# Kernel tuning notes

Hardware: AMD Instinct MI355X
Metric: run time of the kernel (lower is better)

## Reference

```python
import jax, jax.numpy as jnp
import numpy as np

NEG = -1e32
EPS_LN = 1e-5

def _layer_norm(x, w, b):
    mu = jnp.mean(x, axis=-1, keepdims=True)
    var = jnp.mean((x - mu) ** 2, axis=-1, keepdims=True)
    return (x - mu) / jnp.sqrt(var + EPS_LN) * w + b

def setup_inputs() -> dict:
    key = jax.random.key(0)
    ks = jax.random.split(key, 10)
    B, S, D, H, F = 2, 2048, 1024, 16, 4096
    s = 0.02
    return {
        "query": jax.random.normal(ks[0], (B, S, D), jnp.float32),
        "key": jax.random.normal(ks[1], (B, S, D), jnp.float32),
        "values": jax.random.normal(ks[2], (B, S, D), jnp.float32),
        "Wk": jax.random.normal(ks[3], (D, D), jnp.float32) * s,
        "bk": jnp.zeros((D,), jnp.float32),
        "Wv": jax.random.normal(ks[4], (D, D), jnp.float32) * s,
        "bv": jnp.zeros((D,), jnp.float32),
        "Wo": jax.random.normal(ks[5], (D, D), jnp.float32) * s,
        "bo": jnp.zeros((D,), jnp.float32),
        "gammas": jax.random.normal(ks[6], (H, 1, 1), jnp.float32),
        "ln1_w": jnp.ones((D,), jnp.float32),
        "ln1_b": jnp.zeros((D,), jnp.float32),
        "W1": jax.random.normal(ks[7], (F, D), jnp.float32) * s,
        "b1": jnp.zeros((F,), jnp.float32),
        "W2": jax.random.normal(ks[8], (D, F), jnp.float32) * s,
        "b2": jnp.zeros((D,), jnp.float32),
        "ln2_w": jnp.ones((D,), jnp.float32),
        "ln2_b": jnp.zeros((D,), jnp.float32),
        "mask": 1,
    }

def _forward(query, key, values, Wk, bk, Wv, bv, Wo, bo, gammas,
             ln1_w, ln1_b, W1, b1, W2, b2, ln2_w, ln2_b, mask):
    B, S, D = query.shape
    H = gammas.shape[0]
    dk = D // H
    # kq_same=True: q and k both use k_linear
    def proj(x, W, b):
        return (x @ W.T + b).reshape(B, S, H, dk).transpose(0, 2, 1, 3)  # bhsd
    q = proj(query, Wk, bk)
    k = proj(key, Wk, bk)
    v = proj(values, Wv, bv)

    scores = jnp.einsum("bhqd,bhkd->bhqk", q, k) / np.sqrt(dk).astype(np.float32)
    # src_mask: np.triu(ones, k=mask)==0 -> allowed where j <= i + mask - 1
    allow = jnp.tril(jnp.ones((S, S), bool), k=mask - 1)[None, None]  # (1,1,S,S)

    # --- distance decay (no_grad block in torch) ---
    scores_ = jax.nn.softmax(jnp.where(allow, scores, NEG), axis=-1)
    scores_ = scores_ * allow.astype(scores_.dtype)
    distcum = jnp.cumsum(scores_, axis=-1)
    disttotal = jnp.sum(scores_, axis=-1, keepdims=True)
    idx = jnp.arange(S)
    position_effect = jnp.abs(idx[:, None] - idx[None, :]).astype(jnp.float32)[None, None]
    dist_scores = jnp.sqrt(jnp.clip((disttotal - distcum) * position_effect, 0.0, None))
    gamma = -jax.nn.softplus(gammas)[None]  # (1,H,1,1)
    total_effect = jnp.clip(jnp.exp(dist_scores * gamma), 1e-5, 1e5)
    total_effect = jax.lax.stop_gradient(total_effect)
    # ---

    scores = scores * total_effect
    scores = jnp.where(allow, scores, NEG)
    attn = jax.nn.softmax(scores, axis=-1)
    out = jnp.einsum("bhqk,bhkd->bhqd", attn, v)
    concat = out.transpose(0, 2, 1, 3).reshape(B, S, D)
    query2 = concat @ Wo.T + bo

    x = _layer_norm(query + query2, ln1_w, ln1_b)
    ff = jax.nn.relu(x @ W1.T + b1) @ W2.T + b2
    x = _layer_norm(x + ff, ln2_w, ln2_b)
    return x

def reference(query, key, values, Wk, bk, Wv, bv, Wo, bo, gammas,
              ln1_w, ln1_b, W1, b1, W2, b2, ln2_w, ln2_b, mask):
    return _forward(query, key, values, Wk, bk, Wv, bv, Wo, bo, gammas,
                    ln1_w, ln1_b, W1, b1, W2, b2, ln2_w, ln2_b, mask)
```

## Files before the change

### kernel.cpp

```cpp
#include <hip/hip_runtime.h>
#include <hip/hip_bf16.h>

#define B_   2
#define S_   2048
#define D_   1024
#define H_   16
#define DK_  64
#define F_   4096
#define M_   (B_*S_)
#define PD   72

typedef __attribute__((ext_vector_type(8))) short short8;
typedef __attribute__((ext_vector_type(4))) float f32x4;

__device__ __forceinline__ float bf2f(unsigned short s) { return __uint_as_float(((unsigned int)s) << 16); }
__device__ __forceinline__ unsigned short f2bf(float f) {
    unsigned int u = __float_as_uint(f);
    u += 0x7fffu + ((u >> 16) & 1u);
    return (unsigned short)(u >> 16);
}

__device__ __forceinline__ bool probe_f32(const unsigned int* p) {
    return *p == 0x3F800000u;
}
__device__ __forceinline__ float ld1e(const void* p, size_t idx, bool f32) {
    return f32 ? ((const float*)p)[idx] : bf2f(((const unsigned short*)p)[idx]);
}
__device__ __forceinline__ void st1e(void* p, size_t idx, bool f32, float v) {
    if (f32) ((float*)p)[idx] = v;
    else     ((unsigned short*)p)[idx] = f2bf(v);
}

__device__ __forceinline__ void async16(void* lds, const void* g) {
    __builtin_amdgcn_global_load_lds(
        (const __attribute__((address_space(1))) void*)g,
        (__attribute__((address_space(3))) void*)lds, 16, 0, 0);
}

__device__ __forceinline__ unsigned int cvt_pk_bf16(float a, float b) {
    unsigned int r;
    asm("v_cvt_pk_bf16_f32 %0, %1, %2" : "=v"(r) : "v"(a), "v"(b));
    return r;
}

template <bool IS_MAX>
__device__ __forceinline__ float block_reduce(float val, float* buf, int tid) {
    buf[tid] = val;
    __syncthreads();
    #pragma unroll
    for (int off = 128; off > 0; off >>= 1) {
        if (tid < off) {
            float o = buf[tid + off];
            buf[tid] = IS_MAX ? fmaxf(buf[tid], o) : (buf[tid] + o);
        }
        __syncthreads();
    }
    float r = buf[0];
    __syncthreads();
    return r;
}

__global__ __launch_bounds__(256) void cvt_all(
    const void* __restrict__ W1, const void* __restrict__ W2,
    const void* __restrict__ Wk, const void* __restrict__ Wv,
    const void* __restrict__ Wo,
    const void* __restrict__ Qi, const void* __restrict__ Ki,
    const void* __restrict__ Vi,
    unsigned short* __restrict__ W1b, unsigned short* __restrict__ W2b,
    unsigned short* __restrict__ Wkb, unsigned short* __restrict__ Wvb,
    unsigned short* __restrict__ Wob,
    unsigned short* __restrict__ qcb, unsigned short* __restrict__ kcb,
    unsigned short* __restrict__ vcb,
    const unsigned int* __restrict__ probe)
{
    const bool p32 = probe_f32(probe);
    const int blk = blockIdx.x;
    const void* src;
    unsigned short* dst;
    int off;
    if (blk < 2048)      { src = W1; dst = W1b; off = blk; }
    else if (blk < 4096) { src = W2; dst = W2b; off = blk - 2048; }
    else if (blk < 4608) { src = Wk; dst = Wkb; off = blk - 4096; }
    else if (blk < 5120) { src = Wv; dst = Wvb; off = blk - 4608; }
    else if (blk < 5632) { src = Wo; dst = Wob; off = blk - 5120; }
    else if (blk < 7680) { if (!p32) return; src = Qi; dst = qcb; off = blk - 5632; }
    else if (blk < 9728) { if (!p32) return; src = Ki; dst = kcb; off = blk - 7680; }
    else                 { if (!p32) return; src = Vi; dst = vcb; off = blk - 9728; }
    const int i8 = (off * 256 + threadIdx.x) * 8;
    if (p32) {
        const float4 a = *(const float4*)((const float*)src + i8);
        const float4 b = *(const float4*)((const float*)src + i8 + 4);
        short8 o;
        o[0] = (short)f2bf(a.x); o[1] = (short)f2bf(a.y);
        o[2] = (short)f2bf(a.z); o[3] = (short)f2bf(a.w);
        o[4] = (short)f2bf(b.x); o[5] = (short)f2bf(b.y);
        o[6] = (short)f2bf(b.z); o[7] = (short)f2bf(b.w);
        *(short8*)(dst + i8) = o;
    } else {
        *(uint4*)(dst + i8) = *(const uint4*)((const unsigned short*)src + i8);
    }
}

template <int RELU, int AEXT, int CEXT>
__device__ __forceinline__ void gemm_body(
    const void* __restrict__ A,
    const unsigned short* __restrict__ W,
    const void* __restrict__ bias,
    void* __restrict__ C,
    int M, int N, int K, bool p32, int bx, int by)
{
    __shared__ unsigned short As[2][128 * 32];
    __shared__ unsigned short Ws[2][128 * 32];

    const bool a32 = AEXT && p32;
    const bool c32 = CEXT && p32;

    const int tid = threadIdx.x;
    const int lane = tid & 63;
    const int w = tid >> 6;
    const int wr = w >> 1;
    const int wc = w & 1;
    const int col16 = lane & 15;
    const int quad = lane >> 4;

    const int m0 = by * 128;
    const int n0 = bx * 128;

    const int c0 = tid, c1 = 256 + tid;
    const int r0 = c0 >> 2, kc0 = (((c0 & 3) ^ ((c0 >> 3) & 3)) * 8);
    const int r1 = c1 >> 2, kc1 = (((c1 & 3) ^ ((c1 >> 3) & 3)) * 8);

    const int fcol = ((quad ^ ((col16 >> 1) & 3)) * 8);

    f32x4 acc[4][4];
    #pragma unroll
    for (int mt = 0; mt < 4; mt++)
        #pragma unroll
        for (int nt = 0; nt < 4; nt++)
            acc[mt][nt] = (f32x4){0.f, 0.f, 0.f, 0.f};

    auto stage = [&](int bb, int k0) {
        async16(&Ws[bb][c0 * 8], W + (size_t)(n0 + r0) * K + k0 + kc0);
        async16(&Ws[bb][c1 * 8], W + (size_t)(n0 + r1) * K + k0 + kc1);
        if (a32) {
            const float* a0 = (const float*)A + (size_t)(m0 + r0) * K + k0 + kc0;
            const float* a1 = (const float*)A + (size_t)(m0 + r1) * K + k0 + kc1;
            const float4 x0 = *(const float4*)a0, y0 = *(const float4*)(a0 + 4);
            const float4 x1 = *(const float4*)a1, y1 = *(const float4*)(a1 + 4);
            short8 s0, s1;
            s0[0] = (short)f2bf(x0.x); s0[1] = (short)f2bf(x0.y);
            s0[2] = (short)f2bf(x0.z); s0[3] = (short)f2bf(x0.w);
            s0[4] = (short)f2bf(y0.x); s0[5] = (short)f2bf(y0.y);
            s0[6] = (short)f2bf(y0.z); s0[7] = (short)f2bf(y0.w);
            s1[0] = (short)f2bf(x1.x); s1[1] = (short)f2bf(x1.y);
            s1[2] = (short)f2bf(x1.z); s1[3] = (short)f2bf(x1.w);
            s1[4] = (short)f2bf(y1.x); s1[5] = (short)f2bf(y1.y);
            s1[6] = (short)f2bf(y1.z); s1[7] = (short)f2bf(y1.w);
            *(short8*)&As[bb][c0 * 8] = s0;
            *(short8*)&As[bb][c1 * 8] = s1;
        } else {
            const unsigned short* Ab = (const unsigned short*)A;
            async16(&As[bb][c0 * 8], Ab + (size_t)(m0 + r0) * K + k0 + kc0);
            async16(&As[bb][c1 * 8], Ab + (size_t)(m0 + r1) * K + k0 + kc1);
        }
    };

    stage(0, 0);
    __syncthreads();
    int cur = 0;
    for (int k0 = 0; k0 < K; k0 += 32) {
        const int nxt = cur ^ 1;
        if (k0 + 32 < K) stage(nxt, k0 + 32);

        short8 av[4], bv[4];
        #pragma unroll
        for (int mt = 0; mt < 4; mt++)
            av[mt] = *(const short8*)&As[cur][(wr * 64 + mt * 16 + col16) * 32 + fcol];
        #pragma unroll
        for (int nt = 0; nt < 4; nt++)
            bv[nt] = *(const short8*)&Ws[cur][(wc * 64 + nt * 16 + col16) * 32 + fcol];
        #pragma unroll
        for (int mt = 0; mt < 4; mt++)
            #pragma unroll
            for (int nt = 0; nt < 4; nt++)
                acc[mt][nt] = __builtin_amdgcn_mfma_f32_16x16x32_bf16(
                    av[mt], bv[nt], acc[mt][nt], 0, 0, 0);
        __syncthreads();
        cur = nxt;
    }

    #pragma unroll
    for (int mt = 0; mt < 4; mt++) {
        const int row = m0 + wr * 64 + mt * 16 + quad * 4;
        #pragma unroll
        for (int nt = 0; nt < 4; nt++) {
            const int col = n0 + wc * 64 + nt * 16 + col16;
            const float bb = ld1e(bias, col, p32);
            #pragma unroll
            for (int r = 0; r < 4; r++) {
                float v = acc[mt][nt][r] + bb;
                if (RELU) v = fmaxf(v, 0.f);
                st1e(C, (size_t)(row + r) * N + col, c32, v);
            }
        }
    }
}

template <int RELU, int AEXT, int CEXT>
__global__ __launch_bounds__(256) void gemm_mf(
    const void* __restrict__ A,
    const unsigned short* __restrict__ W,
    const void* __restrict__ bias,
    void* __restrict__ C,
    int M, int N, int K,
    const unsigned int* __restrict__ probe)
{
    gemm_body<RELU, AEXT, CEXT>(A, W, bias, C, M, N, K, probe_f32(probe),
                                blockIdx.x, blockIdx.y);
}

template <int RELU, int CEXT>
__global__ __launch_bounds__(1024) void gemm_sk(
    const unsigned short* __restrict__ A,
    const unsigned short* __restrict__ W,
    const void* __restrict__ bias,
    void* __restrict__ C,
    int M, int N, int K,
    const unsigned int* __restrict__ probe)
{
    __shared__ unsigned short SS[4][2][2][128 * 32];
    float* const R0 = (float*)&SS[0][0][0][0];
    float* const R1 = (float*)&SS[2][0][0][0];

    const bool p32 = probe_f32(probe);
    const bool c32 = CEXT && p32;

    const int tid = threadIdx.x;
    const int g = tid >> 8;
    const int tl = tid & 255;
    const int lane = tl & 63;
    const int w = tl >> 6;
    const int wr = w >> 1;
    const int wc = w & 1;
    const int col16 = lane & 15;
    const int quad = lane >> 4;

    const int m0 = blockIdx.y * 128;
    const int n0 = blockIdx.x * 128;

    const int c0 = tl, c1 = 256 + tl;
    const int r0 = c0 >> 2, kc0 = (((c0 & 3) ^ ((c0 >> 3) & 3)) * 8);
    const int r1 = c1 >> 2, kc1 = (((c1 & 3) ^ ((c1 >> 3) & 3)) * 8);
    const int fcol = ((quad ^ ((col16 >> 1) & 3)) * 8);

    const int Kq = K >> 2;
    const int kbeg = g * Kq;

    f32x4 acc[4][4];
    #pragma unroll
    for (int mt = 0; mt < 4; mt++)
        #pragma unroll
        for (int nt = 0; nt < 4; nt++)
            acc[mt][nt] = (f32x4){0.f, 0.f, 0.f, 0.f};

    auto stage = [&](int bb, int k0) {
        async16(&SS[g][bb][1][c0 * 8], W + (size_t)(n0 + r0) * K + k0 + kc0);
        async16(&SS[g][bb][1][c1 * 8], W + (size_t)(n0 + r1) * K + k0 + kc1);
        async16(&SS[g][bb][0][c0 * 8], A + (size_t)(m0 + r0) * K + k0 + kc0);
        async16(&SS[g][bb][0][c1 * 8], A + (size_t)(m0 + r1) * K + k0 + kc1);
    };

    stage(0, kbeg);
    __syncthreads();
    int cur = 0;
    for (int kk = 0; kk < Kq; kk += 32) {
        const int nxt = cur ^ 1;
        if (kk + 32 < Kq) stage(nxt, kbeg + kk + 32);

        short8 av[4], bv[4];
        #pragma unroll
        for (int mt = 0; mt < 4; mt++)
            av[mt] = *(const short8*)&SS[g][cur][0][(wr * 64 + mt * 16 + col16) * 32 + fcol];
        #pragma unroll
        for (int nt = 0; nt < 4; nt++)
            bv[nt] = *(const short8*)&SS[g][cur][1][(wc * 64 + nt * 16 + col16) * 32 + fcol];
        #pragma unroll
        for (int mt = 0; mt < 4; mt++)
            #pragma unroll
            for (int nt = 0; nt < 4; nt++)
                acc[mt][nt] = __builtin_amdgcn_mfma_f32_16x16x32_bf16(
                    av[mt], bv[nt], acc[mt][nt], 0, 0, 0);
        __syncthreads();
        cur = nxt;
    }

    if (g == 1 || g == 3) {
        float* R = (g == 1) ? R0 : R1;
        #pragma unroll
        for (int mt = 0; mt < 4; mt++)
            #pragma unroll
            for (int nt = 0; nt < 4; nt++) {
                const int lrow = wr * 64 + mt * 16 + quad * 4;
                const int lcol = wc * 64 + nt * 16 + col16;
                #pragma unroll
                for (int r = 0; r < 4; r++)
                    R[(lrow + r) * 128 + lcol] = acc[mt][nt][r];
            }
    }
    __syncthreads();
    if (g == 0 || g == 2) {
        const float* R = (g == 0) ? R0 : R1;
        #pragma unroll
        for (int mt = 0; mt < 4; mt++)
            #pragma unroll
            for (int nt = 0; nt < 4; nt++) {
                const int lrow = wr * 64 + mt * 16 + quad * 4;
                const int lcol = wc * 64 + nt * 16 + col16;
                #pragma unroll
                for (int r = 0; r < 4; r++)
                    acc[mt][nt][r] += R[(lrow + r) * 128 + lcol];
            }
    }
    __syncthreads();
    if (g == 2) {
        #pragma unroll
        for (int mt = 0; mt < 4; mt++)
            #pragma unroll
            for (int nt = 0; nt < 4; nt++) {
                const int lrow = wr * 64 + mt * 16 + quad * 4;
                const int lcol = wc * 64 + nt * 16 + col16;
                #pragma unroll
                for (int r = 0; r < 4; r++)
                    R0[(lrow + r) * 128 + lcol] = acc[mt][nt][r];
            }
    }
    __syncthreads();
    if (g == 0) {
        #pragma unroll
        for (int mt = 0; mt < 4; mt++) {
            const int lrow = wr * 64 + mt * 16 + quad * 4;
            const int row = m0 + lrow;
            #pragma unroll
            for (int nt = 0; nt < 4; nt++) {
                const int lcol = wc * 64 + nt * 16 + col16;
                const int col = n0 + lcol;
                const float bb = ld1e(bias, col, p32);
                #pragma unroll
                for (int r = 0; r < 4; r++) {
                    float v = acc[mt][nt][r] + R0[(lrow + r) * 128 + lcol] + bb;
                    if (RELU) v = fmaxf(v, 0.f);
                    st1e(C, (size_t)(row + r) * N + col, c32, v);
                }
            }
        }
    }
}

__global__ __launch_bounds__(256) void gemm_proj(
    const void* __restrict__ q_orig, const void* __restrict__ k_orig,
    const void* __restrict__ v_orig,
    const unsigned short* __restrict__ qcb, const unsigned short* __restrict__ kcb,
    const unsigned short* __restrict__ vcb,
    const unsigned short* __restrict__ Wkb, const unsigned short* __restrict__ Wvb,
    const void* __restrict__ bk, const void* __restrict__ bv,
    unsigned short* __restrict__ qw, unsigned short* __restrict__ kw,
    unsigned short* __restrict__ vw,
    const unsigned int* __restrict__ probe)
{
    const bool p32 = probe_f32(probe);
    const int z = blockIdx.z;
    const unsigned short* W = (z == 2) ? Wvb : Wkb;
    const void* bias = (z == 2) ? bv : bk;
    void* C = (z == 0) ? (void*)qw : (z == 1) ? (void*)kw : (void*)vw;
    if (z == 2 && p32 && vcb == nullptr) {
        gemm_body<0, 1, 0>(v_orig, W, bias, C, M_, D_, D_, p32,
                           blockIdx.x, blockIdx.y);
    } else {
        const void* A = (z == 0) ? (p32 ? (const void*)qcb : q_orig)
                      : (z == 1) ? (p32 ? (const void*)kcb : k_orig)
                                 : (p32 ? (const void*)vcb : v_orig);
        gemm_body<0, 0, 0>(A, W, bias, C, M_, D_, D_, p32,
                           blockIdx.x, blockIdx.y);
    }
}

__global__ __launch_bounds__(256) void vtrans(
    const unsigned short* __restrict__ vw,
    unsigned short* __restrict__ vtg)
{
    __shared__ unsigned short T[64 * PD];
    const int tid = threadIdx.x;
    const int bid = blockIdx.x;
    const int bh = bid & 31;
    const int kt = bid >> 5;
    const int h = bh & 15, b = bh >> 4;
    #pragma unroll
    for (int cc = 0; cc < 2; cc++) {
        const int c = tid + cc * 256;
        const int key = c >> 3, dc = c & 7;
        const uint4 u = *(const uint4*)(vw + (size_t)(b * S_ + kt * 64 + key) * D_ + h * 64 + dc * 8);
        unsigned short* dst = &T[(dc * 8) * PD + key];
        dst[0 * PD] = (unsigned short)(u.x & 0xffff);
        dst[1 * PD] = (unsigned short)(u.x >> 16);
        dst[2 * PD] = (unsigned short)(u.y & 0xffff);
        dst[3 * PD] = (unsigned short)(u.y >> 16);
        dst[4 * PD] = (unsigned short)(u.z & 0xffff);
        dst[5 * PD] = (unsigned short)(u.z >> 16);
        dst[6 * PD] = (unsigned short)(u.w & 0xffff);
        dst[7 * PD] = (unsigned short)(u.w >> 16);
    }
    __syncthreads();
    #pragma unroll
    for (int cc = 0; cc < 2; cc++) {
        const int c = tid + cc * 256;
        const int d = c >> 3, kc = c & 7;
        const uint4 u = *(const uint4*)&T[d * PD + kc * 8];
        *(uint4*)(vtg + ((size_t)bh * 64 + d) * S_ + kt * 64 + kc * 8) = u;
    }
}

__global__ __launch_bounds__(256) void attn_mfma(
    const unsigned short* __restrict__ qw,
    const unsigned short* __restrict__ kw,
    const unsigned short* __restrict__ vtg,
    const void* __restrict__ gam,
    const int* __restrict__ maskp,
    unsigned short* __restrict__ outc,
    const unsigned int* __restrict__ probe)
{
    __shared__ unsigned short Qs[64 * PD];
    __shared__ unsigned short Ks[64 * PD];
    __shared__ unsigned short Vt[64 * PD];
    unsigned int* const Pu = (unsigned int*)Qs;

    const bool p32 = probe_f32(probe);
    const int tid = threadIdx.x;
    const int lane = tid & 63;
    const int w = tid >> 6;
    const int col16 = lane & 15;
    const int quad = lane >> 4;
    const int bid = blockIdx.x;
    const int qt = 31 - (bid >> 5);
    const int bh = bid & 31;
    const int h = bh & 15;
    const int b = bh >> 4;
    const int i0 = qt * 64;

    const int mask = *maskp;
    long long nje = (long long)i0 + 63 + (long long)mask;
    int njmax = (nje > S_) ? S_ : (int)nje;
    if (njmax < 1) njmax = 1;
    const int ntiles = (njmax + 63) >> 6;
    long long fm = (long long)i0 + (long long)mask - 64;
    int nfull = 0;
    if (fm >= 0) {
        long long v = (fm >> 6) + 1;
        nfull = (v > ntiles) ? ntiles : (int)v;
    }

    const float L2E = 1.44269504088896f;
    const float gval = ld1e(gam, h, p32);
    const float sp = (gval > 20.f) ? gval : log1pf(__expf(gval));
    const float g2 = -sp * L2E;
    const float SC2 = 0.125f * L2E;

    const int myrow = i0 + w * 16 + col16;
    const int limq = myrow + mask - quad * 4;

    #pragma unroll
    for (int cc = 0; cc < 2; cc++) {
        const int c = tid + cc * 256;
        const int row = c >> 3, dc = c & 7;
        const uint4 u = *(const uint4*)(qw + (size_t)(b * S_ + i0 + row) * D_ + h * 64 + dc * 8);
        *(uint4*)&Qs[row * PD + dc * 8] = u;
    }
    __syncthreads();

    short8 avq[2];
    #pragma unroll
    for (int ks = 0; ks < 2; ks++)
        avq[ks] = *(const short8*)&Qs[(w * 16 + col16) * PD + ks * 32 + quad * 8];

    float T1l = 0.f;
    for (int t = 0; t < ntiles; t++) {
        const int j0 = t * 64;
        __syncthreads();
        #pragma unroll
        for (int cc = 0; cc < 2; cc++) {
            const int c = tid + cc * 256;
            const int row = c >> 3, dc = c & 7;
            const uint4 u = *(const uint4*)(kw + (size_t)(b * S_ + j0 + row) * D_ + h * 64 + dc * 8);
            *(uint4*)&Ks[row * PD + dc * 8] = u;
        }
        __syncthreads();

        f32x4 acc[4];
        #pragma unroll
        for (int nt = 0; nt < 4; nt++) acc[nt] = (f32x4){0.f, 0.f, 0.f, 0.f};
        #pragma unroll
        for (int ks = 0; ks < 2; ks++)
            #pragma unroll
            for (int nt = 0; nt < 4; nt++) {
                const short8 kv = *(const short8*)&Ks[(nt * 16 + col16) * PD + ks * 32 + quad * 8];
                acc[nt] = __builtin_amdgcn_mfma_f32_16x16x32_bf16(kv, avq[ks], acc[nt], 0, 0, 0);
            }

        if (t >= nfull) {
            #pragma unroll
            for (int nt = 0; nt < 4; nt++) {
                const int Ln = limq - j0 - nt * 16;
                #pragma unroll
                for (int r = 0; r < 4; r++)
                    acc[nt][r] = (r < Ln) ? acc[nt][r] : -3.0e38f;
            }
        }

        #pragma unroll
        for (int nt = 0; nt < 4; nt++)
            #pragma unroll
            for (int r = 0; r < 4; r++)
                T1l += __builtin_amdgcn_exp2f(acc[nt][r] * SC2);
    }
    T1l += __shfl_xor(T1l, 16, 64);
    T1l += __shfl_xor(T1l, 32, 64);
    const float rT1 = 1.0f / T1l;

    float l2 = 0.f;
    float Cb_run = 0.f;
    f32x4 O[4];
    #pragma unroll
    for (int nt = 0; nt < 4; nt++) O[nt] = (f32x4){0.f, 0.f, 0.f, 0.f};

    for (int t = 0; t < ntiles; t++) {
        const int j0 = t * 64;
        __syncthreads();
        #pragma unroll
        for (int cc = 0; cc < 2; cc++) {
            const int c = tid + cc * 256;
            const int row = c >> 3, dc = c & 7;
            const uint4 u = *(const uint4*)(kw + (size_t)(b * S_ + j0 + row) * D_ + h * 64 + dc * 8);
            *(uint4*)&Ks[row * PD + dc * 8] = u;
        }
        #pragma unroll
        for (int cc = 0; cc < 2; cc++) {
            const int c = tid + cc * 256;
            const int d = c >> 3, kc = c & 7;
            const uint4 u = *(const uint4*)(vtg + ((size_t)bh * 64 + d) * S_ + j0 + kc * 8);
            *(uint4*)&Vt[d * PD + kc * 8] = u;
        }
        __syncthreads();

        f32x4 acc[4];
        #pragma unroll
        for (int nt = 0; nt < 4; nt++) acc[nt] = (f32x4){0.f, 0.f, 0.f, 0.f};
        #pragma unroll
        for (int ks = 0; ks < 2; ks++)
            #pragma unroll
            for (int nt = 0; nt < 4; nt++) {
                const short8 kv = *(const short8*)&Ks[(nt * 16 + col16) * PD + ks * 32 + quad * 8];
                acc[nt] = __builtin_amdgcn_mfma_f32_16x16x32_bf16(kv, avq[ks], acc[nt], 0, 0, 0);
            }

        if (t >= nfull) {
            #pragma unroll
            for (int nt = 0; nt < 4; nt++) {
                const int Ln = limq - j0 - nt * 16;
                #pragma unroll
                for (int r = 0; r < 4; r++)
                    acc[nt][r] = (r < Ln) ? acc[nt][r] : -3.0e38f;
            }
        }

        float s2v[4][4], loc[4][4], run4[4];
        #pragma unroll
        for (int nt = 0; nt < 4; nt++) {
            float rr = 0.f;
            #pragma unroll
            for (int r = 0; r < 4; r++) {
                const float s2 = acc[nt][r] * SC2;
                s2v[nt][r] = s2;
                rr += __builtin_amdgcn_exp2f(s2);
                loc[nt][r] = rr;
            }
            run4[nt] = rr;
        }
        float excl[4], tot[4];
        #pragma unroll
        for (int nt = 0; nt < 4; nt++) {
            float v = run4[nt];
            const float u1 = __shfl_up(v, 16, 64); if (quad >= 1) v += u1;
            const float u2 = __shfl_up(v, 32, 64); if (quad >= 2) v += u2;
            excl[nt] = v - run4[nt];
            tot[nt] = __shfl(v, col16 + 48, 64);
        }

        float Cb = Cb_run;
        #pragma unroll
        for (int nt = 0; nt < 4; nt++) {
            const float CeR = (Cb + excl[nt]) * rT1;
            const float d0f = (float)(myrow - j0 - nt * 16 - quad * 4);
            float p4[4];
            #pragma unroll
            for (int r = 0; r < 4; r++) {
                const float cumn = __builtin_fmaf(loc[nt][r], rT1, CeR);
                const float rem = fmaxf(1.f - cumn, 0.f);
                const float pe = fabsf(d0f - (float)r);
                const float te = fmaxf(
                    __builtin_amdgcn_exp2f(g2 * __builtin_amdgcn_sqrtf(rem * pe)), 1e-5f);
                const float tv = s2v[nt][r] * te;
                p4[r] = __builtin_amdgcn_exp2f(tv);
                l2 += p4[r];
            }
            uint2 pk;
            pk.x = cvt_pk_bf16(p4[0], p4[1]);
            pk.y = cvt_pk_bf16(p4[2], p4[3]);
            *(uint2*)&Pu[(w * 16 + col16) * 36 + nt * 8 + quad * 2] = pk;
            Cb += tot[nt];
        }
        Cb_run = Cb;

        const short8 pa0 = *(const short8*)&Pu[(w * 16 + col16) * 36 + 0 * 16 + quad * 4];
        const short8 pa1 = *(const short8*)&Pu[(w * 16 + col16) * 36 + 1 * 16 + quad * 4];
        #pragma unroll
        for (int nt = 0; nt < 4; nt++) {
            const short8 bv0 = *(const short8*)&Vt[(nt * 16 + col16) * PD + 0 * 32 + quad * 8];
            const short8 bv1 = *(const short8*)&Vt[(nt * 16 + col16) * PD + 1 * 32 + quad * 8];
            O[nt] = __builtin_amdgcn_mfma_f32_16x16x32_bf16(pa0, bv0, O[nt], 0, 0, 0);
            O[nt] = __builtin_amdgcn_mfma_f32_16x16x32_bf16(pa1, bv1, O[nt], 0, 0, 0);
        }
    }

    l2 += __shfl_xor(l2, 16, 64);
    l2 += __shfl_xor(l2, 32, 64);
    const float rl2 = 1.0f / l2;
    float rl2O[4];
    #pragma unroll
    for (int r = 0; r < 4; r++) rl2O[r] = __shfl(rl2, quad * 4 + r, 64);
    #pragma unroll
    for (int nt = 0; nt < 4; nt++)
        #pragma unroll
        for (int r = 0; r < 4; r++)
            outc[(size_t)(b * S_ + i0 + w * 16 + quad * 4 + r) * D_ + h * 64 + nt * 16 + col16] =
                f2bf(O[nt][r] * rl2O[r]);
}

__global__ __launch_bounds__(256) void ln_fused(
    const void* __restrict__ A,
    const void* __restrict__ Bq,
    const void* __restrict__ w,
    const void* __restrict__ bias,
    void* __restrict__ out,
    const unsigned int* __restrict__ probe, int aext, int bext, int oext)
{
    __shared__ float xs[D_];
    __shared__ float red[256];
    const bool p32 = probe_f32(probe);
    const bool a32 = aext && p32;
    const bool b32 = bext && p32;
    const bool o32 = oext && p32;

    const int tid = threadIdx.x;
    const size_t row = (size_t)blockIdx.x * D_;

    float lsum = 0.f;
    #pragma unroll
    for (int qq = 0; qq < 4; qq++) {
        const int j = tid + qq * 256;
        const float x = ld1e(A, row + j, a32) + ld1e(Bq, row + j, b32);
        xs[j] = x;
        lsum += x;
    }
    const float mu = block_reduce<false>(lsum, red, tid) * (1.0f / D_);

    float lv = 0.f;
    #pragma unroll
    for (int qq = 0; qq < 4; qq++) {
        const int j = tid + qq * 256;
        const float dd = xs[j] - mu;
        lv += dd * dd;
    }
    const float var = block_reduce<false>(lv, red, tid) * (1.0f / D_);
    const float rs = rsqrtf(var + 1e-5f);

    #pragma unroll
    for (int qq = 0; qq < 4; qq++) {
        const int j = tid + qq * 256;
        const float o = (xs[j] - mu) * rs * ld1e(w, j, p32) + ld1e(bias, j, p32);
        st1e(out, row + j, o32, o);
    }
}

extern "C" void kernel_launch(void* const* d_in, const int* in_sizes, int n_in,
                              void* d_out, int out_size, void* d_ws, size_t ws_size,
                              hipStream_t stream)
{
    (void)in_sizes; (void)n_in; (void)out_size;

    const void* query  = d_in[0];
    const void* key_   = d_in[1];
    const void* values = d_in[2];
    const void* Wk     = d_in[3];
    const void* bk     = d_in[4];
    const void* Wv     = d_in[5];
    const void* bv     = d_in[6];
    const void* Wo     = d_in[7];
    const void* bo     = d_in[8];
    const void* gammas = d_in[9];
    const void* ln1w   = d_in[10];
    const void* ln1b   = d_in[11];
    const void* W1     = d_in[12];
    const void* b1     = d_in[13];
    const void* W2     = d_in[14];
    const void* b2     = d_in[15];
    const void* ln2w   = d_in[16];
    const void* ln2b   = d_in[17];
    const int*  maskp  = (const int*)d_in[18];
    const unsigned int* probe = (const unsigned int*)ln1w;

    char* ws = (char*)d_ws;
    const size_t MiB = 1024 * 1024;
    unsigned short* W1b = (unsigned short*)(ws + 0 * MiB);
    unsigned short* W2b = (unsigned short*)(ws + 8 * MiB);
    unsigned short* Wkb = (unsigned short*)(ws + 16 * MiB);
    unsigned short* Wvb = (unsigned short*)(ws + 18 * MiB);
    unsigned short* Wob = (unsigned short*)(ws + 20 * MiB);
    unsigned short* qw  = (unsigned short*)(ws + 22 * MiB);
    unsigned short* kw  = (unsigned short*)(ws + 30 * MiB);
    unsigned short* vw  = (unsigned short*)(ws + 38 * MiB);
    unsigned short* cw  = (unsigned short*)(ws + 46 * MiB);
    unsigned short* vtg = (unsigned short*)(ws + 54 * MiB);
    unsigned short* x1  = (unsigned short*)(ws + 22 * MiB);
    unsigned short* fh  = (unsigned short*)(ws + 30 * MiB);
    unsigned short* qc  = (unsigned short*)(ws + 46 * MiB);
    unsigned short* kc  = (unsigned short*)(ws + 54 * MiB);
    unsigned short* vc  = (ws_size >= (size_t)70 * MiB)
                          ? (unsigned short*)(ws + 62 * MiB) : nullptr;

    const dim3 blk(256);
    const dim3 blk10(1024);
    const int cvtgrid = vc ? 11776 : 9728;
    cvt_all<<<dim3(cvtgrid), blk, 0, stream>>>(
        W1, W2, Wk, Wv, Wo, query, key_, values,
        W1b, W2b, Wkb, Wvb, Wob, qc, kc, vc, probe);
    gemm_proj<<<dim3(D_ / 128, M_ / 128, 3), blk, 0, stream>>>(
        query, key_, values, qc, kc, vc, Wkb, Wvb, bk, bv, qw, kw, vw, probe);
    vtrans<<<dim3(1024), blk, 0, stream>>>(vw, vtg);
    attn_mfma<<<dim3(B_ * H_ * (S_ / 64)), blk, 0, stream>>>(
        qw, kw, vtg, gammas, maskp, cw, probe);
    gemm_sk<0, 0><<<dim3(D_ / 128, M_ / 128), blk10, 0, stream>>>(
        cw, Wob, bo, x1, M_, D_, D_, probe);
    ln_fused<<<dim3(M_), blk, 0, stream>>>(query, x1, ln1w, ln1b, x1, probe, 1, 0, 0);
    gemm_mf<1, 0, 0><<<dim3(F_ / 128, M_ / 128), blk, 0, stream>>>(
        x1, W1b, b1, fh, M_, F_, D_, probe);
    gemm_sk<0, 1><<<dim3(D_ / 128, M_ / 128), blk10, 0, stream>>>(
        fh, W2b, b2, d_out, M_, D_, F_, probe);
    ln_fused<<<dim3(M_), blk, 0, stream>>>(x1, d_out, ln2w, ln2b, d_out, probe, 0, 1, 1);
}
```

Measured before the change: 454.4 us.

## Replace split-K 1024-thread GEMM with 128x64-tile 256-thread GEMM

The split-K GEMM, with four 256-thread groups each reducing a quarter of K and combining partials through LDS, is replaced by a plain GEMM with 128x64 output tiles and 256 threads. The grid doubles along N to keep parallelism, so there are 512 blocks for the M=4096, N=1024 output projection and FFN down-projection. This removes the LDS reduction passes and extra barriers and lowers per-block resource use. In exchange each block runs the full K loop serially (up to 4096 for W2), and the A tile is reloaded by twice as many column blocks.

```diff
diff --git a/kernel.cpp b/kernel.cpp
--- a/kernel.cpp
+++ b/kernel.cpp
@@ -220,7 +220,7 @@
 }
 
 template <int RELU, int CEXT>
-__global__ __launch_bounds__(1024) void gemm_sk(
+__global__ __launch_bounds__(256) void gemm_n64(
     const unsigned short* __restrict__ A,
     const unsigned short* __restrict__ W,
     const void* __restrict__ bias,
@@ -228,64 +228,56 @@
     int M, int N, int K,
     const unsigned int* __restrict__ probe)
 {
-    __shared__ unsigned short SS[4][2][2][128 * 32];
-    float* const R0 = (float*)&SS[0][0][0][0];
-    float* const R1 = (float*)&SS[2][0][0][0];
+    __shared__ unsigned short As[2][128 * 32];
+    __shared__ unsigned short Ws[2][64 * 32];
 
     const bool p32 = probe_f32(probe);
     const bool c32 = CEXT && p32;
 
     const int tid = threadIdx.x;
-    const int g = tid >> 8;
-    const int tl = tid & 255;
-    const int lane = tl & 63;
-    const int w = tl >> 6;
-    const int wr = w >> 1;
-    const int wc = w & 1;
+    const int lane = tid & 63;
+    const int w = tid >> 6;
     const int col16 = lane & 15;
     const int quad = lane >> 4;
 
     const int m0 = blockIdx.y * 128;
-    const int n0 = blockIdx.x * 128;
-
-    const int c0 = tl, c1 = 256 + tl;
+    const int n0 = blockIdx.x * 64;
+
+    const int c0 = tid, c1 = 256 + tid;
     const int r0 = c0 >> 2, kc0 = (((c0 & 3) ^ ((c0 >> 3) & 3)) * 8);
     const int r1 = c1 >> 2, kc1 = (((c1 & 3) ^ ((c1 >> 3) & 3)) * 8);
+    const int rw = tid >> 2, kcw = (((tid & 3) ^ ((tid >> 3) & 3)) * 8);
     const int fcol = ((quad ^ ((col16 >> 1) & 3)) * 8);
 
-    const int Kq = K >> 2;
-    const int kbeg = g * Kq;
-
-    f32x4 acc[4][4];
-    #pragma unroll
-    for (int mt = 0; mt < 4; mt++)
+    f32x4 acc[2][4];
+    #pragma unroll
+    for (int mt = 0; mt < 2; mt++)
         #pragma unroll
         for (int nt = 0; nt < 4; nt++)
             acc[mt][nt] = (f32x4){0.f, 0.f, 0.f, 0.f};
 
     auto stage = [&](int bb, int k0) {
-        async16(&SS[g][bb][1][c0 * 8], W + (size_t)(n0 + r0) * K + k0 + kc0);
-        async16(&SS[g][bb][1][c1 * 8], W + (size_t)(n0 + r1) * K + k0 + kc1);
-        async16(&SS[g][bb][0][c0 * 8], A + (size_t)(m0 + r0) * K + k0 + kc0);
-        async16(&SS[g][bb][0][c1 * 8], A + (size_t)(m0 + r1) * K + k0 + kc1);
+        async16(&Ws[bb][tid * 8], W + (size_t)(n0 + rw) * K + k0 + kcw);
+        async16(&As[bb][c0 * 8], A + (size_t)(m0 + r0) * K + k0 + kc0);
+        async16(&As[bb][c1 * 8], A + (size_t)(m0 + r1) * K + k0 + kc1);
     };
 
-    stage(0, kbeg);
+    stage(0, 0);
     __syncthreads();
     int cur = 0;
-    for (int kk = 0; kk < Kq; kk += 32) {
+    for (int k0 = 0; k0 < K; k0 += 32) {
         const int nxt = cur ^ 1;
-        if (kk + 32 < Kq) stage(nxt, kbeg + kk + 32);
-
-        short8 av[4], bv[4];
-        #pragma unroll
-        for (int mt = 0; mt < 4; mt++)
-            av[mt] = *(const short8*)&SS[g][cur][0][(wr * 64 + mt * 16 + col16) * 32 + fcol];
+        if (k0 + 32 < K) stage(nxt, k0 + 32);
+
+        short8 av[2], bv[4];
+        #pragma unroll
+        for (int mt = 0; mt < 2; mt++)
+            av[mt] = *(const short8*)&As[cur][(w * 32 + mt * 16 + col16) * 32 + fcol];
         #pragma unroll
         for (int nt = 0; nt < 4; nt++)
-            bv[nt] = *(const short8*)&SS[g][cur][1][(wc * 64 + nt * 16 + col16) * 32 + fcol];
-        #pragma unroll
-        for (int mt = 0; mt < 4; mt++)
+            bv[nt] = *(const short8*)&Ws[cur][(nt * 16 + col16) * 32 + fcol];
+        #pragma unroll
+        for (int mt = 0; mt < 2; mt++)
             #pragma unroll
             for (int nt = 0; nt < 4; nt++)
                 acc[mt][nt] = __builtin_amdgcn_mfma_f32_16x16x32_bf16(
@@ -294,63 +286,18 @@
         cur = nxt;
     }
 
-    if (g == 1 || g == 3) {
-        float* R = (g == 1) ? R0 : R1;
-        #pragma unroll
-        for (int mt = 0; mt < 4; mt++)
-            #pragma unroll
-            for (int nt = 0; nt < 4; nt++) {
-                const int lrow = wr * 64 + mt * 16 + quad * 4;
-                const int lcol = wc * 64 + nt * 16 + col16;
-                #pragma unroll
-                for (int r = 0; r < 4; r++)
-                    R[(lrow + r) * 128 + lcol] = acc[mt][nt][r];
-            }
-    }
-    __syncthreads();
-    if (g == 0 || g == 2) {
-        const float* R = (g == 0) ? R0 : R1;
-        #pragma unroll
-        for (int mt = 0; mt < 4; mt++)
-            #pragma unroll
-            for (int nt = 0; nt < 4; nt++) {
-                const int lrow = wr * 64 + mt * 16 + quad * 4;
-                const int lcol = wc * 64 + nt * 16 + col16;
-                #pragma unroll
-                for (int r = 0; r < 4; r++)
-                    acc[mt][nt][r] += R[(lrow + r) * 128 + lcol];
-            }
-    }
-    __syncthreads();
-    if (g == 2) {
-        #pragma unroll
-        for (int mt = 0; mt < 4; mt++)
-            #pragma unroll
-            for (int nt = 0; nt < 4; nt++) {
-                const int lrow = wr * 64 + mt * 16 + quad * 4;
-                const int lcol = wc * 64 + nt * 16 + col16;
-                #pragma unroll
-                for (int r = 0; r < 4; r++)
-                    R0[(lrow + r) * 128 + lcol] = acc[mt][nt][r];
-            }
-    }
-    __syncthreads();
-    if (g == 0) {
-        #pragma unroll
-        for (int mt = 0; mt < 4; mt++) {
-            const int lrow = wr * 64 + mt * 16 + quad * 4;
-            const int row = m0 + lrow;
-            #pragma unroll
-            for (int nt = 0; nt < 4; nt++) {
-                const int lcol = wc * 64 + nt * 16 + col16;
-                const int col = n0 + lcol;
-                const float bb = ld1e(bias, col, p32);
-                #pragma unroll
-                for (int r = 0; r < 4; r++) {
-                    float v = acc[mt][nt][r] + R0[(lrow + r) * 128 + lcol] + bb;
-                    if (RELU) v = fmaxf(v, 0.f);
-                    st1e(C, (size_t)(row + r) * N + col, c32, v);
-                }
+    #pragma unroll
+    for (int mt = 0; mt < 2; mt++) {
+        const int row = m0 + w * 32 + mt * 16 + quad * 4;
+        #pragma unroll
+        for (int nt = 0; nt < 4; nt++) {
+            const int col = n0 + nt * 16 + col16;
+            const float bb = ld1e(bias, col, p32);
+            #pragma unroll
+            for (int r = 0; r < 4; r++) {
+                float v = acc[mt][nt][r] + bb;
+                if (RELU) v = fmaxf(v, 0.f);
+                st1e(C, (size_t)(row + r) * N + col, c32, v);
             }
         }
     }
@@ -737,7 +684,6 @@
                           ? (unsigned short*)(ws + 62 * MiB) : nullptr;
 
     const dim3 blk(256);
-    const dim3 blk10(1024);
     const int cvtgrid = vc ? 11776 : 9728;
     cvt_all<<<dim3(cvtgrid), blk, 0, stream>>>(
         W1, W2, Wk, Wv, Wo, query, key_, values,
@@ -747,12 +693,12 @@
     vtrans<<<dim3(1024), blk, 0, stream>>>(vw, vtg);
     attn_mfma<<<dim3(B_ * H_ * (S_ / 64)), blk, 0, stream>>>(
         qw, kw, vtg, gammas, maskp, cw, probe);
-    gemm_sk<0, 0><<<dim3(D_ / 128, M_ / 128), blk10, 0, stream>>>(
+    gemm_n64<0, 0><<<dim3(D_ / 64, M_ / 128), blk, 0, stream>>>(
         cw, Wob, bo, x1, M_, D_, D_, probe);
     ln_fused<<<dim3(M_), blk, 0, stream>>>(query, x1, ln1w, ln1b, x1, probe, 1, 0, 0);
     gemm_mf<1, 0, 0><<<dim3(F_ / 128, M_ / 128), blk, 0, stream>>>(
         x1, W1b, b1, fh, M_, F_, D_, probe);
-    gemm_sk<0, 1><<<dim3(D_ / 128, M_ / 128), blk10, 0, stream>>>(
+    gemm_n64<0, 1><<<dim3(D_ / 64, M_ / 128), blk, 0, stream>>>(
         fh, W2b, b2, d_out, M_, D_, F_, probe);
     ln_fused<<<dim3(M_), blk, 0, stream>>>(x1, d_out, ln2w, ln2b, d_out, probe, 0, 1, 1);
 }
```

Result: slower. 466.5 us (+2.7%).
